# Optimization experiments

Measured on AMD Instinct MI355X. Metric: run time of the kernel, lower is better.

Reference implementation:

```python
import jax, jax.numpy as jnp
import numpy as np

B, C, IMG, P = 64, 3, 224, 16
D, L, H, DH, M, NC = 768, 12, 12, 64, 3072, 1000
INNER = H * DH
PD = C * P * P          # patch_dim = 768
NP = (IMG // P) ** 2    # 196 patches


def setup_inputs() -> dict:
    key = jax.random.key(0)
    ks = jax.random.split(key, 16)
    s = 0.02
    nrm = lambda k, shape: jax.random.normal(k, shape, jnp.float32) * s
    return dict(
        img=jax.random.normal(ks[0], (B, C, IMG, IMG), jnp.float32),
        patch_ln1_g=jnp.ones(PD), patch_ln1_b=jnp.zeros(PD),
        patch_w=nrm(ks[1], (PD, D)), patch_b=jnp.zeros(D),
        patch_ln2_g=jnp.ones(D), patch_ln2_b=jnp.zeros(D),
        pos_emb=nrm(ks[2], (1, NP + 1, D)),
        cls_tok=nrm(ks[3], (1, 1, D)),
        attn_ln_g=jnp.ones((L, D)), attn_ln_b=jnp.zeros((L, D)),
        w_qkv=nrm(ks[4], (L, D, 3 * INNER)),
        w_out=nrm(ks[5], (L, INNER, D)), b_out=jnp.zeros((L, D)),
        ff_ln_g=jnp.ones((L, D)), ff_ln_b=jnp.zeros((L, D)),
        ff_w1=nrm(ks[6], (L, D, M)), ff_b1=jnp.zeros((L, M)),
        ff_w2=nrm(ks[7], (L, M, D)), ff_b2=jnp.zeros((L, D)),
        final_ln_g=jnp.ones(D), final_ln_b=jnp.zeros(D),
        head_w=nrm(ks[8], (D, NC)), head_b=jnp.zeros(NC),
    )


def _ln(x, g, b, eps=1e-5):
    m = x.mean(-1, keepdims=True)
    v = ((x - m) ** 2).mean(-1, keepdims=True)
    return (x - m) / jnp.sqrt(v + eps) * g + b


def reference(img, patch_ln1_g, patch_ln1_b, patch_w, patch_b, patch_ln2_g,
              patch_ln2_b, pos_emb, cls_tok, attn_ln_g, attn_ln_b, w_qkv,
              w_out, b_out, ff_ln_g, ff_ln_b, ff_w1, ff_b1, ff_w2, ff_b2,
              final_ln_g, final_ln_b, head_w, head_b):
    b, c, hh, ww = img.shape
    h, w = hh // P, ww // P
    # Rearrange 'b c (h p1) (w p2) -> b (h w) (p1 p2 c)'
    x = img.reshape(b, c, h, P, w, P).transpose(0, 2, 4, 3, 5, 1).reshape(b, h * w, P * P * c)
    x = _ln(x, patch_ln1_g, patch_ln1_b)
    x = x @ patch_w + patch_b
    x = _ln(x, patch_ln2_g, patch_ln2_b)
    n = x.shape[1]
    x = jnp.concatenate([jnp.broadcast_to(cls_tok, (b, 1, x.shape[-1])), x], axis=1)
    x = x + pos_emb[:, : n + 1]
    scale = DH ** -0.5
    for l in range(L):
        xn = _ln(x, attn_ln_g[l], attn_ln_b[l])
        qkv = xn @ w_qkv[l]  # [b, n+1, 3*inner]
        q, k, v = jnp.split(qkv, 3, axis=-1)
        sp = lambda t: t.reshape(b, -1, H, DH).transpose(0, 2, 1, 3)  # b h n d
        q, k, v = sp(q), sp(k), sp(v)
        # softmax variant: exp(scores*scale), normalize by sum + eps (no max-subtract, faithful to source)
        numer = jnp.exp(jnp.einsum('bhid,bhjd->bhij', q, k) * scale)
        attn = numer / (numer.sum(-1, keepdims=True) + 1e-8)
        out = jnp.einsum('bhij,bhjd->bhid', attn, v)
        out = out.transpose(0, 2, 1, 3).reshape(b, -1, INNER)
        x = out @ w_out[l] + b_out[l] + x
        xn = _ln(x, ff_ln_g[l], ff_ln_b[l])
        hid = jax.nn.gelu(xn @ ff_w1[l] + ff_b1[l], approximate=False)
        x = hid @ ff_w2[l] + ff_b2[l] + x
    x = _ln(x, final_ln_g, final_ln_b)
    return x[:, 0] @ head_w + head_b
```

## Files before the change

### kernel.cpp

```cpp
#include <hip/hip_runtime.h>
#include <hip/hip_bf16.h>
#include <math.h>

#define B_     64
#define NTOK   197
#define NPATCH 196
#define D768   768
#define NL     12
#define NH     12
#define MFF    3072
#define NCLS   1000
#define ROWS   (B_ * NTOK)
#define PROWS  (B_ * NPATCH)
#define ROWS_PAD 12672

typedef unsigned short ushort;
typedef __bf16 bf16x8 __attribute__((ext_vector_type(8)));
typedef float  f32x4  __attribute__((ext_vector_type(4)));
typedef unsigned short u16x4 __attribute__((ext_vector_type(4)));
typedef unsigned short u16x2 __attribute__((ext_vector_type(2)));

__device__ __forceinline__ ushort f2b(float f) {
  __hip_bfloat16 h = __float2bfloat16(f);
  return *reinterpret_cast<ushort*>(&h);
}
__device__ __forceinline__ float b2f(ushort u) {
  unsigned int v = ((unsigned int)u) << 16;
  float f;
  __builtin_memcpy(&f, &v, 4);
  return f;
}

__device__ __forceinline__ void gload16(const ushort* g, ushort* lds) {
  __builtin_amdgcn_global_load_lds((const __attribute__((address_space(1))) void*)g,
                                   (__attribute__((address_space(3))) void*)lds, 16, 0, 0);
}

__device__ __forceinline__ float gelu_f(float v) {
  float t = v * fmaf(0.0713548162726f, v * v, 1.5957691216f);
  return v / (1.0f + __expf(-t));
}

__device__ __forceinline__ void block_mean_rstd(float s, float sq, float& mean, float& rstd) {
#pragma unroll
  for (int off = 32; off; off >>= 1) { s += __shfl_xor(s, off); sq += __shfl_xor(sq, off); }
  __shared__ float ss[4], ssq[4];
  int w = threadIdx.x >> 6;
  if ((threadIdx.x & 63) == 0) { ss[w] = s; ssq[w] = sq; }
  __syncthreads();
  s  = ss[0] + ss[1] + ss[2] + ss[3];
  sq = ssq[0] + ssq[1] + ssq[2] + ssq[3];
  mean = s * (1.0f / 768.0f);
  float var = sq * (1.0f / 768.0f) - mean * mean;
  rstd = rsqrtf(var + 1e-5f);
}

__global__ __launch_bounds__(256) void ln_rows4(const ushort* __restrict__ in, long in_stride,
                                                const float* __restrict__ g,
                                                const float* __restrict__ bta,
                                                ushort* __restrict__ out) {
  const int w = threadIdx.x >> 6, l = threadIdx.x & 63;
  const size_t row = (size_t)blockIdx.x * 4 + w;
  const ushort* xr = in + row * in_stride;
  u16x4 xv[3];
  xv[0] = *(const u16x4*)(xr + l * 4);
  xv[1] = *(const u16x4*)(xr + 256 + l * 4);
  xv[2] = *(const u16x4*)(xr + 512 + l * 4);
  float v[12];
  float s = 0.f, sq = 0.f;
#pragma unroll
  for (int i = 0; i < 3; ++i)
#pragma unroll
    for (int j = 0; j < 4; ++j) {
      float f = b2f(xv[i][j]);
      v[i * 4 + j] = f;
      s += f; sq += f * f;
    }
#pragma unroll
  for (int off = 32; off; off >>= 1) { s += __shfl_xor(s, off); sq += __shfl_xor(sq, off); }
  float mean = s * (1.0f / 768.0f);
  float rstd = rsqrtf(sq * (1.0f / 768.0f) - mean * mean + 1e-5f);
  ushort* o = out + row * 768;
#pragma unroll
  for (int i = 0; i < 3; ++i) {
    int base = i * 256 + l * 4;
    f32x4 gv = *(const f32x4*)(g + base);
    f32x4 bv = *(const f32x4*)(bta + base);
    u16x4 ov = { f2b((v[i*4+0] - mean) * rstd * gv[0] + bv[0]),
                 f2b((v[i*4+1] - mean) * rstd * gv[1] + bv[1]),
                 f2b((v[i*4+2] - mean) * rstd * gv[2] + bv[2]),
                 f2b((v[i*4+3] - mean) * rstd * gv[3] + bv[3]) };
    *(u16x4*)(o + base) = ov;
  }
}

__global__ __launch_bounds__(256) void patch_ln1(const float* __restrict__ img,
                                                 const float* __restrict__ g,
                                                 const float* __restrict__ bta,
                                                 ushort* __restrict__ xp) {
  int pidx = blockIdx.x;
  int b = pidx / NPATCH, hw = pidx % NPATCH;
  int ph = hw / 14, pw = hw % 14;
  int t = threadIdx.x;
  float v[3];
#pragma unroll
  for (int u = 0; u < 3; ++u) {
    int k = t + u * 256;
    int c = k % 3, p2 = (k / 3) & 15, p1 = k / 48;
    v[u] = img[(((size_t)b * 3 + c) * 224 + ph * 16 + p1) * 224 + pw * 16 + p2];
  }
  float mean, rstd;
  block_mean_rstd(v[0] + v[1] + v[2], v[0] * v[0] + v[1] * v[1] + v[2] * v[2], mean, rstd);
  ushort* o = xp + (size_t)pidx * 768;
#pragma unroll
  for (int u = 0; u < 3; ++u) { int k = t + u * 256; o[k] = f2b((v[u] - mean) * rstd * g[k] + bta[k]); }
}

__global__ __launch_bounds__(256) void ln2_pos(const float* __restrict__ xe,
                                               const float* __restrict__ g,
                                               const float* __restrict__ bta,
                                               const float* __restrict__ pos,
                                               ushort* __restrict__ x) {
  int pidx = blockIdx.x;
  int b = pidx / NPATCH, i = pidx % NPATCH;
  const float* xr = xe + (size_t)pidx * 768;
  int t = threadIdx.x;
  float v0 = xr[t], v1 = xr[t + 256], v2 = xr[t + 512];
  float mean, rstd;
  block_mean_rstd(v0 + v1 + v2, v0 * v0 + v1 * v1 + v2 * v2, mean, rstd);
  const float* p = pos + (size_t)(1 + i) * 768;
  ushort* o = x + ((size_t)b * NTOK + 1 + i) * 768;
  o[t]       = f2b((v0 - mean) * rstd * g[t]       + bta[t]       + p[t]);
  o[t + 256] = f2b((v1 - mean) * rstd * g[t + 256] + bta[t + 256] + p[t + 256]);
  o[t + 512] = f2b((v2 - mean) * rstd * g[t + 512] + bta[t + 512] + p[t + 512]);
}

__global__ __launch_bounds__(256) void cls_init(const float* __restrict__ cls_tok,
                                                const float* __restrict__ pos,
                                                ushort* __restrict__ x) {
  int b = blockIdx.x, t = threadIdx.x;
  ushort* o = x + (size_t)b * NTOK * 768;
#pragma unroll
  for (int u = 0; u < 3; ++u) { int k = t + u * 256; o[k] = f2b(cls_tok[k] + pos[k]); }
}

__global__ __launch_bounds__(256) void transpose_cast(const float* __restrict__ W,
                                                      ushort* __restrict__ Wt,
                                                      int K, int N) {
  __shared__ float t[32][33];
  int n0 = blockIdx.x * 32, k0 = blockIdx.y * 32;
  int tx = threadIdx.x, ty = threadIdx.y;
#pragma unroll
  for (int u = 0; u < 32; u += 8) {
    int n = n0 + tx;
    t[ty + u][tx] = (n < N) ? W[(size_t)(k0 + ty + u) * N + n] : 0.f;
  }
  __syncthreads();
#pragma unroll
  for (int u = 0; u < 32; u += 8) {
    int n = n0 + ty + u;
    if (n < N) Wt[(size_t)n * K + k0 + tx] = f2b(t[tx][ty + u]);
  }
}

__device__ __forceinline__ void transpose_layer64(int bid,
                                                  const float* wq, const float* wo,
                                                  const float* w1, const float* w2,
                                                  ushort* tq, ushort* to,
                                                  ushort* t1, ushort* t2) {
  const float* W; ushort* Wt; int K, N, xt;
  if (bid < 432)       {             W = wq; Wt = tq; K = 768;  N = 2304; xt = 36; }
  else if (bid < 576)  { bid -= 432; W = wo; Wt = to; K = 768;  N = 768;  xt = 12; }
  else if (bid < 1152) { bid -= 576; W = w1; Wt = t1; K = 768;  N = 3072; xt = 48; }
  else                 { bid -= 1152; W = w2; Wt = t2; K = 3072; N = 768; xt = 12; }
  int n0 = (bid % xt) * 64, k0 = (bid / xt) * 64;
  __shared__ float t[64][65];
  int id = threadIdx.x;
  int tx = id & 15, ty = id >> 4;
#pragma unroll
  for (int u = 0; u < 4; ++u) {
    int k = ty + 16 * u;
    f32x4 v = *(const f32x4*)(W + (size_t)(k0 + k) * N + n0 + tx * 4);
    t[k][tx * 4 + 0] = v[0]; t[k][tx * 4 + 1] = v[1];
    t[k][tx * 4 + 2] = v[2]; t[k][tx * 4 + 3] = v[3];
  }
  __syncthreads();
  int wx = id & 31, wy = id >> 5;
#pragma unroll
  for (int u = 0; u < 8; ++u) {
    int n = wy + 8 * u;
    u16x2 o = { f2b(t[wx * 2][n]), f2b(t[wx * 2 + 1][n]) };
    *(u16x2*)(Wt + (size_t)(n0 + n) * K + k0 + wx * 2) = o;
  }
}

__global__ __launch_bounds__(256) void transpose4(const float* __restrict__ wq,
                                                  const float* __restrict__ wo,
                                                  const float* __restrict__ w1,
                                                  const float* __restrict__ w2,
                                                  ushort* __restrict__ tq,
                                                  ushort* __restrict__ to,
                                                  ushort* __restrict__ t1,
                                                  ushort* __restrict__ t2) {
  transpose_layer64(blockIdx.x, wq, wo, w1, w2, tq, to, t1, t2);
}

__global__ __launch_bounds__(256) void transpose_all(const float* __restrict__ wq,
                                                     const float* __restrict__ wo,
                                                     const float* __restrict__ w1,
                                                     const float* __restrict__ w2,
                                                     ushort* __restrict__ tq,
                                                     ushort* __restrict__ to,
                                                     ushort* __restrict__ t1,
                                                     ushort* __restrict__ t2) {
  int l = blockIdx.x / 1728, bid = blockIdx.x % 1728;
  transpose_layer64(bid,
                    wq + (size_t)l * 768 * 2304, wo + (size_t)l * 768 * 768,
                    w1 + (size_t)l * 768 * MFF,  w2 + (size_t)l * MFF * 768,
                    tq + (size_t)l * 2304 * 768, to + (size_t)l * 768 * 768,
                    t1 + (size_t)l * MFF * 768,  t2 + (size_t)l * 768 * MFF);
}

template<int EP, int RESID, int OBF>
__global__ __launch_bounds__(256, 4) void gemm_v6(const ushort* __restrict__ A,
                                                  const ushort* __restrict__ Bt,
                                                  const float* __restrict__ bias,
                                                  const void* __restrict__ resid,
                                                  void* __restrict__ Cv,
                                                  int M, int N, int K) {
  __shared__ ushort smem[2 * 8192];

  const int tid = threadIdx.x;
  const int w = tid >> 6, l = tid & 63;
  const int fr = l & 15, fc = l >> 4;

  const int ntx = gridDim.x;
  const int nwg = ntx * gridDim.y;
  const int orig = blockIdx.y * ntx + blockIdx.x;
  const int q = nwg >> 3, r = nwg & 7, xcd = orig & 7, idx = orig >> 3;
  const int wg = (xcd < r ? xcd * (q + 1) : r * (q + 1) + (xcd - r) * q) + idx;
  const int row0 = (wg / ntx) * 128, col0 = (wg % ntx) * 128;

  const int wr = (w >> 1) * 64, wc = (w & 1) * 64;

  const int srow = tid >> 2;
  const int sg = (tid & 3) ^ ((srow >> 1) & 3);
  const ushort* pA0 = A  + (size_t)(row0 + srow) * K + sg * 8;
  const ushort* pA1 = A  + (size_t)(row0 + 64 + srow) * K + sg * 8;
  const ushort* pB0 = Bt + (size_t)(col0 + srow) * K + sg * 8;
  const ushort* pB1 = Bt + (size_t)(col0 + 64 + srow) * K + sg * 8;

  auto stage = [&](int t_, ushort* dst) {
    const int k0 = t_ * 32;
    gload16(pA0 + k0, dst + tid * 8);
    gload16(pA1 + k0, dst + (tid + 256) * 8);
    gload16(pB0 + k0, dst + 4096 + tid * 8);
    gload16(pB1 + k0, dst + 4096 + (tid + 256) * 8);
  };

  int idxA[4], idxB[4];
#pragma unroll
  for (int m = 0; m < 4; ++m) {
    int rA = wr + m * 16 + fr;
    idxA[m] = rA * 32 + ((fc ^ ((rA >> 1) & 3)) << 3);
  }
#pragma unroll
  for (int n = 0; n < 4; ++n) {
    int rB = wc + n * 16 + fr;
    idxB[n] = rB * 32 + ((fc ^ ((rB >> 1) & 3)) << 3);
  }

  f32x4 acc[4][4] = {};

  auto compute = [&](const ushort* As) {
    const ushort* Bs = As + 4096;
    bf16x8 a_[4], b_[4];
#pragma unroll
    for (int m = 0; m < 4; ++m) a_[m] = *(const bf16x8*)(As + idxA[m]);
#pragma unroll
    for (int n = 0; n < 4; ++n) b_[n] = *(const bf16x8*)(Bs + idxB[n]);
#pragma unroll
    for (int m = 0; m < 4; ++m)
#pragma unroll
      for (int n = 0; n < 4; ++n)
        acc[m][n] = __builtin_amdgcn_mfma_f32_16x16x32_bf16(b_[n], a_[m], acc[m][n], 0, 0, 0);
  };

#define VM4() asm volatile("s_waitcnt vmcnt(4)" ::: "memory")
#define VM0() asm volatile("s_waitcnt vmcnt(0)" ::: "memory")

  const int NT = K >> 5;

  stage(0, smem);
  for (int t = 0; t < NT; t += 2) {
    if (t + 1 < NT) { stage(t + 1, smem + 8192); VM4(); } else VM0();
    __builtin_amdgcn_s_barrier();
    compute(smem);
    __builtin_amdgcn_s_barrier();
    if (t + 1 < NT) {
      if (t + 2 < NT) { stage(t + 2, smem); VM4(); } else VM0();
      __builtin_amdgcn_s_barrier();
      compute(smem + 8192);
      __builtin_amdgcn_s_barrier();
    }
  }
#undef VM4
#undef VM0

  if (!OBF) {
    float* Cf = (float*)Cv;
#pragma unroll
    for (int m = 0; m < 4; ++m) {
      int row = row0 + wr + m * 16 + fr;
      if (row >= M) continue;
#pragma unroll
      for (int n = 0; n < 4; ++n) {
        int col = col0 + wc + n * 16 + fc * 4;
        f32x4 v = acc[m][n];
        if (bias) v += *(const f32x4*)(bias + col);
        if (EP) {
#pragma unroll
          for (int rr = 0; rr < 4; ++rr) v[rr] = gelu_f(v[rr]);
        }
        if (RESID) v += *(const f32x4*)((const float*)resid + (size_t)row * N + col);
        *(f32x4*)(Cf + (size_t)row * N + col) = v;
      }
    }
  } else {
    __syncthreads();
    ushort* Cw = smem + w * 4096;
#pragma unroll
    for (int m = 0; m < 4; ++m) {
      int rl = m * 16 + fr;
      int row = row0 + wr + rl;
#pragma unroll
      for (int n = 0; n < 4; ++n) {
        int col = col0 + wc + n * 16 + fc * 4;
        f32x4 v = acc[m][n];
        if (bias) v += *(const f32x4*)(bias + col);
        if (EP) {
#pragma unroll
          for (int rr = 0; rr < 4; ++rr) v[rr] = gelu_f(v[rr]);
        }
        if (RESID) {
          u16x4 rv = *(const u16x4*)((const ushort*)resid + (size_t)row * N + col);
#pragma unroll
          for (int rr = 0; rr < 4; ++rr) v[rr] += b2f(rv[rr]);
        }
        u16x4 pk = { f2b(v[0]), f2b(v[1]), f2b(v[2]), f2b(v[3]) };
        int s = (n * 4 + fc) ^ (rl & 7);
        *(u16x4*)(Cw + rl * 64 + s * 4) = pk;
      }
    }
    ushort* Cb = (ushort*)Cv;
#pragma unroll
    for (int pp = 0; pp < 16; ++pp) {
      int rl = pp * 4 + (l >> 4);
      int cs = l & 15;
      u16x4 pk = *(const u16x4*)(Cw + rl * 64 + ((cs ^ (rl & 7)) * 4));
      int row = row0 + wr + rl;
      if (row < M) *(u16x4*)(Cb + (size_t)row * N + col0 + wc + cs * 4) = pk;
    }
  }
}

template<int EP, int RESID, int OBF>
__global__ __launch_bounds__(256) void gemm_bt(const ushort* __restrict__ A,
                                               const ushort* __restrict__ Bt,
                                               const float* __restrict__ bias,
                                               const float* __restrict__ resid,
                                               void* __restrict__ C,
                                               int M, int N, int K) {
  __shared__ ushort As[128 * 32];
  __shared__ ushort Bs[128 * 32];
  int tid = threadIdx.x;
  int w = tid >> 6, l = tid & 63;
  int fr = l & 15, fc = l >> 4;
  int row0 = blockIdx.y * 128, col0 = blockIdx.x * 128;
  int wr = (w >> 1) * 64, wc = (w & 1) * 64;

  int srow0 = w * 32 + (l >> 2);
  int srow1 = srow0 + 16;
  int sc0 = (((l & 3) ^ ((srow0 >> 1) & 3)) << 3);
  int sc1 = (((l & 3) ^ ((srow1 >> 1) & 3)) << 3);
  const ushort* ga0 = A  + (size_t)(row0 + srow0) * K + sc0;
  const ushort* ga1 = A  + (size_t)(row0 + srow1) * K + sc1;
  const ushort* gb0 = Bt + (size_t)(col0 + srow0) * K + sc0;
  const ushort* gb1 = Bt + (size_t)(col0 + srow1) * K + sc1;

  int idxA[4], idxB[4];
#pragma unroll
  for (int m = 0; m < 4; ++m) {
    int rA = wr + m * 16 + fr;
    idxA[m] = rA * 32 + ((fc ^ ((rA >> 1) & 3)) << 3);
  }
#pragma unroll
  for (int n = 0; n < 4; ++n) {
    int rB = wc + n * 16 + fr;
    idxB[n] = rB * 32 + ((fc ^ ((rB >> 1) & 3)) << 3);
  }

  f32x4 acc[4][4] = {};

  for (int k0 = 0; k0 < K; k0 += 32) {
    gload16(ga0 + k0, &As[w * 1024]);
    gload16(ga1 + k0, &As[w * 1024 + 512]);
    gload16(gb0 + k0, &Bs[w * 1024]);
    gload16(gb1 + k0, &Bs[w * 1024 + 512]);
    __syncthreads();
    bf16x8 af[4], bfr[4];
#pragma unroll
    for (int m = 0; m < 4; ++m) af[m] = *(const bf16x8*)(As + idxA[m]);
#pragma unroll
    for (int n = 0; n < 4; ++n) bfr[n] = *(const bf16x8*)(Bs + idxB[n]);
#pragma unroll
    for (int m = 0; m < 4; ++m)
#pragma unroll
      for (int n = 0; n < 4; ++n)
        acc[m][n] = __builtin_amdgcn_mfma_f32_16x16x32_bf16(af[m], bfr[n], acc[m][n], 0, 0, 0);
    __syncthreads();
  }

#pragma unroll
  for (int n = 0; n < 4; ++n) {
    int col = col0 + wc + n * 16 + fr;
    if (col >= N) continue;
    float bv = bias ? bias[col] : 0.f;
#pragma unroll
    for (int m = 0; m < 4; ++m) {
#pragma unroll
      for (int rr = 0; rr < 4; ++rr) {
        int row = row0 + wr + m * 16 + fc * 4 + rr;
        if (row >= M) continue;
        float v = acc[m][n][rr] + bv;
        if (EP == 1) v = 0.5f * v * (1.0f + erff(v * 0.70710678118654752f));
        if (RESID) v += resid[(size_t)row * N + col];
        if (OBF) ((ushort*)C)[(size_t)row * N + col] = f2b(v);
        else     ((float*)C)[(size_t)row * N + col]  = v;
      }
    }
  }
}

__global__ __launch_bounds__(256) void attn_mfma(const ushort* __restrict__ qkv,
                                                 ushort* __restrict__ aout) {
  int bid = blockIdx.x;
  int qt = bid & 3;
  int h  = (bid >> 2) % NH;
  int b  = (bid >> 2) / NH;
  int tid = threadIdx.x, w = tid >> 6, l = tid & 63;
  int fr = l & 15, fc = l >> 4;

  __shared__ ushort Vt[64 * 64];
  __shared__ ushort Pl[4 * 16 * 64];

  const size_t brow = (size_t)b * NTOK;
  int q0 = qt * 64 + w * 16;

  bf16x8 qf[2];
  {
    const ushort* qp = qkv + (brow + q0 + fr) * 2304 + h * 64 + fc * 8;
    qf[0] = *(const bf16x8*)qp;
    qf[1] = *(const bf16x8*)(qp + 32);
  }
  float rs[4] = {0.f, 0.f, 0.f, 0.f};
  f32x4 oc[4] = {};

  for (int kt = 0; kt < 4; ++kt) {
    __syncthreads();
    {
      int key = tid >> 2, d0 = (tid & 3) * 16;
      int j = kt * 64 + key;
      bool valid = j < NTOK;
      const ushort* vp = qkv + (brow + j) * 2304 + 1536 + h * 64 + d0;
      ushort vbuf[16];
      if (valid) {
        *(bf16x8*)(vbuf)     = *(const bf16x8*)vp;
        *(bf16x8*)(vbuf + 8) = *(const bf16x8*)(vp + 8);
      } else {
#pragma unroll
        for (int i = 0; i < 16; ++i) vbuf[i] = 0;
      }
#pragma unroll
      for (int i = 0; i < 16; ++i) {
        int d = d0 + i;
        int byte = d * 128 + ((((key >> 3)) ^ (d & 7)) << 4) + (key & 7) * 2;
        Vt[byte >> 1] = vbuf[i];
      }
    }
    f32x4 sc[4];
#pragma unroll
    for (int n = 0; n < 4; ++n) {
      f32x4 z = {};
      const ushort* kp = qkv + (brow + kt * 64 + n * 16 + fr) * 2304 + 768 + h * 64 + fc * 8;
      bf16x8 k0 = *(const bf16x8*)kp;
      bf16x8 k1 = *(const bf16x8*)(kp + 32);
      z = __builtin_amdgcn_mfma_f32_16x16x32_bf16(qf[0], k0, z, 0, 0, 0);
      z = __builtin_amdgcn_mfma_f32_16x16x32_bf16(qf[1], k1, z, 0, 0, 0);
      sc[n] = z;
    }
    float part[4] = {0.f, 0.f, 0.f, 0.f};
#pragma unroll
    for (int n = 0; n < 4; ++n) {
      int j = kt * 64 + n * 16 + fr;
      bool jv = j < NTOK;
#pragma unroll
      for (int rr = 0; rr < 4; ++rr) {
        float e = jv ? __expf(sc[n][rr] * 0.125f) : 0.f;
        part[rr] += e;
        int row = fc * 4 + rr, col = n * 16 + fr;
        int byte = row * 128 + (((col >> 3) ^ (row & 7)) << 4) + (col & 7) * 2;
        Pl[w * 1024 + (byte >> 1)] = f2b(e);
      }
    }
#pragma unroll
    for (int rr = 0; rr < 4; ++rr) {
      float p = part[rr];
      p += __shfl_xor(p, 1); p += __shfl_xor(p, 2);
      p += __shfl_xor(p, 4); p += __shfl_xor(p, 8);
      rs[rr] += p;
    }
    __syncthreads();
#pragma unroll
    for (int ks = 0; ks < 2; ++ks) {
      int prow = fr;
      int pbyte = prow * 128 + (((ks * 4 + fc) ^ (prow & 7)) << 4);
      bf16x8 pf = *(const bf16x8*)(Pl + w * 1024 + (pbyte >> 1));
#pragma unroll
      for (int n = 0; n < 4; ++n) {
        int d = n * 16 + fr;
        int vb = d * 128 + (((ks * 4 + fc) ^ (d & 7)) << 4);
        bf16x8 vf = *(const bf16x8*)(Vt + (vb >> 1));
        oc[n] = __builtin_amdgcn_mfma_f32_16x16x32_bf16(pf, vf, oc[n], 0, 0, 0);
      }
    }
  }
#pragma unroll
  for (int n = 0; n < 4; ++n) {
#pragma unroll
    for (int rr = 0; rr < 4; ++rr) {
      int qq = q0 + fc * 4 + rr;
      if (qq < NTOK) {
        float v = oc[n][rr] / (rs[rr] + 1e-8f);
        aout[(brow + qq) * 768 + h * 64 + n * 16 + fr] = f2b(v);
      }
    }
  }
}

extern "C" void kernel_launch(void* const* d_in, const int* in_sizes, int n_in,
                              void* d_out, int out_size, void* d_ws, size_t ws_size,
                              hipStream_t stream) {
  const float* img       = (const float*)d_in[0];
  const float* p_ln1_g   = (const float*)d_in[1];
  const float* p_ln1_b   = (const float*)d_in[2];
  const float* patch_w   = (const float*)d_in[3];
  const float* patch_b   = (const float*)d_in[4];
  const float* p_ln2_g   = (const float*)d_in[5];
  const float* p_ln2_b   = (const float*)d_in[6];
  const float* pos_emb   = (const float*)d_in[7];
  const float* cls_tok   = (const float*)d_in[8];
  const float* attn_ln_g = (const float*)d_in[9];
  const float* attn_ln_b = (const float*)d_in[10];
  const float* w_qkv     = (const float*)d_in[11];
  const float* w_out     = (const float*)d_in[12];
  const float* b_out     = (const float*)d_in[13];
  const float* ff_ln_g   = (const float*)d_in[14];
  const float* ff_ln_b   = (const float*)d_in[15];
  const float* ff_w1     = (const float*)d_in[16];
  const float* ff_b1     = (const float*)d_in[17];
  const float* ff_w2     = (const float*)d_in[18];
  const float* ff_b2     = (const float*)d_in[19];
  const float* fin_ln_g  = (const float*)d_in[20];
  const float* fin_ln_b  = (const float*)d_in[21];
  const float* head_w    = (const float*)d_in[22];
  const float* head_b    = (const float*)d_in[23];
  float* out = (float*)d_out;

  char* p = (char*)d_ws;
  auto alloc = [&](size_t bytes) { char* r = p; p += (bytes + 255) & ~(size_t)255; return r; };
  ushort* x      = (ushort*)alloc((size_t)ROWS_PAD * 768 * 2);
  ushort* xnb    = (ushort*)alloc((size_t)ROWS_PAD * 768 * 2);
  ushort* qkvb   = (ushort*)alloc((size_t)ROWS_PAD * 2304 * 2);
  ushort* aoutb  = (ushort*)alloc((size_t)ROWS_PAD * 768 * 2);
  ushort* pwt    = (ushort*)alloc((size_t)768 * 768 * 2);
  ushort* hwt    = (ushort*)alloc((size_t)1024 * 768 * 2);
  ushort* xclsb  = (ushort*)alloc((size_t)128 * 768 * 2);
  ushort* hidb   = qkvb;
  ushort* xpb    = xnb;
  float*  xe     = (float*)qkvb;

  const size_t SQ = (size_t)2304 * 768, SO = (size_t)768 * 768, S1 = (size_t)MFF * 768;
  size_t used = (size_t)(p - (char*)d_ws);
  bool oneshot = (used + 12 * (SQ + SO + 2 * S1) * 2 + 4096) <= ws_size;
  int nw = oneshot ? 12 : 1;
  ushort* wtq = (ushort*)alloc(nw * SQ * 2);
  ushort* wto = (ushort*)alloc(nw * SO * 2);
  ushort* wt1 = (ushort*)alloc(nw * S1 * 2);
  ushort* wt2 = (ushort*)alloc(nw * S1 * 2);

  dim3 blk(256), tblk(32, 8);

  transpose_cast<<<dim3(24, 24), tblk, 0, stream>>>(patch_w, pwt, 768, 768);
  transpose_cast<<<dim3(32, 24), tblk, 0, stream>>>(head_w, hwt, 768, 1000);
  if (oneshot)
    transpose_all<<<12 * 1728, blk, 0, stream>>>(w_qkv, w_out, ff_w1, ff_w2,
                                                 wtq, wto, wt1, wt2);
  patch_ln1<<<PROWS, blk, 0, stream>>>(img, p_ln1_g, p_ln1_b, xpb);
  gemm_v6<0, 0, 0><<<dim3(6, 98), blk, 0, stream>>>(xpb, pwt, patch_b, nullptr, xe,
                                                    PROWS, 768, 768);
  ln2_pos<<<PROWS, blk, 0, stream>>>(xe, p_ln2_g, p_ln2_b, pos_emb, x);
  cls_init<<<B_, blk, 0, stream>>>(cls_tok, pos_emb, x);

  for (int l = 0; l < NL; ++l) {
    ushort* tq = wtq + (oneshot ? (size_t)l * SQ : 0);
    ushort* to = wto + (oneshot ? (size_t)l * SO : 0);
    ushort* t1 = wt1 + (oneshot ? (size_t)l * S1 : 0);
    ushort* t2 = wt2 + (oneshot ? (size_t)l * S1 : 0);
    if (!oneshot)
      transpose4<<<1728, blk, 0, stream>>>(w_qkv + (size_t)l * 768 * 2304,
                                           w_out + (size_t)l * 768 * 768,
                                           ff_w1 + (size_t)l * 768 * MFF,
                                           ff_w2 + (size_t)l * MFF * 768,
                                           tq, to, t1, t2);

    ln_rows4<<<ROWS / 4, blk, 0, stream>>>(x, 768, attn_ln_g + (size_t)l * 768,
                                           attn_ln_b + (size_t)l * 768, xnb);
    gemm_v6<0, 0, 1><<<dim3(18, 99), blk, 0, stream>>>(xnb, tq, nullptr, nullptr, qkvb,
                                                       ROWS, 2304, 768);
    attn_mfma<<<B_ * NH * 4, blk, 0, stream>>>(qkvb, aoutb);
    gemm_v6<0, 1, 1><<<dim3(6, 99), blk, 0, stream>>>(aoutb, to, b_out + (size_t)l * 768,
                                                      x, x, ROWS, 768, 768);
    ln_rows4<<<ROWS / 4, blk, 0, stream>>>(x, 768, ff_ln_g + (size_t)l * 768,
                                           ff_ln_b + (size_t)l * 768, xnb);
    gemm_v6<1, 0, 1><<<dim3(24, 99), blk, 0, stream>>>(xnb, t1, ff_b1 + (size_t)l * MFF,
                                                       nullptr, hidb, ROWS, MFF, 768);
    gemm_v6<0, 1, 1><<<dim3(6, 99), blk, 0, stream>>>(hidb, t2, ff_b2 + (size_t)l * 768,
                                                      x, x, ROWS, 768, MFF);
  }

  ln_rows4<<<B_ / 4, blk, 0, stream>>>(x, (long)NTOK * 768, fin_ln_g, fin_ln_b, xclsb);
  gemm_bt<0, 0, 0><<<dim3(8, 1), blk, 0, stream>>>(xclsb, hwt, head_b, nullptr, out,
                                                   B_, NCLS, 768);
}
```

Baseline: 4.159 ms.

## Stage attention K tiles in LDS, remap attention blocks, coalesce patch loads

The attention kernel now loads each 64-key K tile into a swizzled LDS buffer using async global-to-LDS loads, then waits on the load counter and syncs. Each wave reads its MFMA K fragments from that shared buffer instead of issuing its own strided global loads. The block index is also remapped so that the four query tiles of groups of eight batch-head pairs are scheduled near each other, which should help L2 reuse. Separately, patch_ln1 is rewritten so each thread reads one pixel per channel from contiguous image rows and writes three interleaved channel outputs. The cost is an extra barrier and extra LDS use in attention, and attention is only a small share of total time.

```diff
diff --git a/kernel.cpp b/kernel.cpp
--- a/kernel.cpp
+++ b/kernel.cpp
@@ -102,18 +102,19 @@
   int b = pidx / NPATCH, hw = pidx % NPATCH;
   int ph = hw / 14, pw = hw % 14;
   int t = threadIdx.x;
+  int p1 = t >> 4, p2 = t & 15;
   float v[3];
 #pragma unroll
-  for (int u = 0; u < 3; ++u) {
-    int k = t + u * 256;
-    int c = k % 3, p2 = (k / 3) & 15, p1 = k / 48;
-    v[u] = img[(((size_t)b * 3 + c) * 224 + ph * 16 + p1) * 224 + pw * 16 + p2];
-  }
+  for (int c = 0; c < 3; ++c)
+    v[c] = img[(((size_t)b * 3 + c) * 224 + ph * 16 + p1) * 224 + pw * 16 + p2];
   float mean, rstd;
   block_mean_rstd(v[0] + v[1] + v[2], v[0] * v[0] + v[1] * v[1] + v[2] * v[2], mean, rstd);
   ushort* o = xp + (size_t)pidx * 768;
 #pragma unroll
-  for (int u = 0; u < 3; ++u) { int k = t + u * 256; o[k] = f2b((v[u] - mean) * rstd * g[k] + bta[k]); }
+  for (int c = 0; c < 3; ++c) {
+    int k = t * 3 + c;
+    o[k] = f2b((v[c] - mean) * rstd * g[k] + bta[k]);
+  }
 }
 
 __global__ __launch_bounds__(256) void ln2_pos(const float* __restrict__ xe,
@@ -444,18 +445,25 @@
 
 __global__ __launch_bounds__(256) void attn_mfma(const ushort* __restrict__ qkv,
                                                  ushort* __restrict__ aout) {
-  int bid = blockIdx.x;
-  int qt = bid & 3;
-  int h  = (bid >> 2) % NH;
-  int b  = (bid >> 2) / NH;
+  int bidp = blockIdx.x;
+  int bh = (bidp & 7) | ((bidp >> 5) << 3);
+  int qt = (bidp >> 3) & 3;
+  int h  = bh % NH;
+  int b  = bh / NH;
   int tid = threadIdx.x, w = tid >> 6, l = tid & 63;
   int fr = l & 15, fc = l >> 4;
 
+  __shared__ ushort Kt[64 * 64];
   __shared__ ushort Vt[64 * 64];
   __shared__ ushort Pl[4 * 16 * 64];
 
   const size_t brow = (size_t)b * NTOK;
   int q0 = qt * 64 + w * 16;
+
+  const int skey = tid >> 3;
+  const int sgk = (tid & 7) ^ ((skey >> 1) & 7);
+  const ushort* pK0 = qkv + (brow + skey) * 2304 + 768 + h * 64 + sgk * 8;
+  const ushort* pK1 = qkv + (brow + 32 + skey) * 2304 + 768 + h * 64 + sgk * 8;
 
   bf16x8 qf[2];
   {
@@ -468,6 +476,11 @@
 
   for (int kt = 0; kt < 4; ++kt) {
     __syncthreads();
+    {
+      const size_t koff = (size_t)kt * 64 * 2304;
+      gload16(pK0 + koff, Kt + tid * 8);
+      gload16(pK1 + koff, Kt + (tid + 256) * 8);
+    }
     {
       int key = tid >> 2, d0 = (tid & 3) * 16;
       int j = kt * 64 + key;
@@ -488,13 +501,17 @@
         Vt[byte >> 1] = vbuf[i];
       }
     }
+    asm volatile("s_waitcnt vmcnt(0)" ::: "memory");
+    __syncthreads();
     f32x4 sc[4];
 #pragma unroll
     for (int n = 0; n < 4; ++n) {
+      int row = n * 16 + fr;
+      int sw = (row >> 1) & 7;
+      const ushort* kr = Kt + row * 64;
+      bf16x8 k0 = *(const bf16x8*)(kr + ((fc ^ sw) << 3));
+      bf16x8 k1 = *(const bf16x8*)(kr + (((fc + 4) ^ sw) << 3));
       f32x4 z = {};
-      const ushort* kp = qkv + (brow + kt * 64 + n * 16 + fr) * 2304 + 768 + h * 64 + fc * 8;
-      bf16x8 k0 = *(const bf16x8*)kp;
-      bf16x8 k1 = *(const bf16x8*)(kp + 32);
       z = __builtin_amdgcn_mfma_f32_16x16x32_bf16(qf[0], k0, z, 0, 0, 0);
       z = __builtin_amdgcn_mfma_f32_16x16x32_bf16(qf[1], k1, z, 0, 0, 0);
       sc[n] = z;
@@ -636,7 +653,7 @@
     gemm_v6<1, 0, 1><<<dim3(24, 99), blk, 0, stream>>>(xnb, t1, ff_b1 + (size_t)l * MFF,
                                                        nullptr, hidb, ROWS, MFF, 768);
     gemm_v6<0, 1, 1><<<dim3(6, 99), blk, 0, stream>>>(hidb, t2, ff_b2 + (size_t)l * 768,
-                                                      x, x, ROWS, 768, MFF);
+                                                      x, x, ROWS, MFF == MFF ? 768 : 768, MFF);
   }
 
   ln_rows4<<<B_ / 4, blk, 0, stream>>>(x, (long)NTOK * 768, fin_ln_g, fin_ln_b, xclsb);
```

Result: faster. 4.038 ms (-2.9%).
